# Kernel optimization log

Measured on AMD Instinct MI355X. Metric: run time of the kernel, lower is better.

Reference implementation:

```python
import jax, jax.numpy as jnp
from jax import lax
import numpy as np

STRIDE = 16
PRE_NMS = 2000
POST_NMS = 300
NMS_THRESH = 0.7
MIN_SIZE = 16.0  # * img_scale (=1.0)
DN = ('NCHW', 'OIHW', 'NCHW')


def _anchor_base(base=16, ratios=(0.5, 1.0, 2.0), scales=(8, 16, 32)):
    py = px = base / 2.0
    ab = np.zeros((len(ratios) * len(scales), 4), np.float32)
    k = 0
    for r in ratios:
        for s in scales:
            h = base * s * np.sqrt(r)
            w = base * s * np.sqrt(1.0 / r)
            ab[k] = [py - h / 2, px - w / 2, py + h / 2, px + w / 2]
            k += 1
    return ab


def _all_anchors(H, W, img_h, img_w):
    base = _anchor_base()
    sy = np.arange(H, dtype=np.float32) * STRIDE
    sx = np.arange(W, dtype=np.float32) * STRIDE
    yy, xx = np.meshgrid(sy, sx, indexing='ij')
    shifts = np.stack([yy, xx, yy, xx], axis=-1).reshape(-1, 1, 4)
    anchors = (shifts + base[None]).reshape(-1, 4).astype(np.float32)  # (H*W*9, 4)
    valid = np.where((anchors[:, 0] >= 0) & (anchors[:, 1] >= 0) &
                     (anchors[:, 2] <= img_h) & (anchors[:, 3] <= img_w))[0]
    return anchors, valid


def _loc2bbox(anc, loc):
    # anc: (1,K,4), loc: (B,K,4); boxes as (y1,x1,y2,x2)
    h = anc[..., 2] - anc[..., 0]
    w = anc[..., 3] - anc[..., 1]
    cy = anc[..., 0] + 0.5 * h
    cx = anc[..., 1] + 0.5 * w
    ncy = loc[..., 0] * h + cy
    ncx = loc[..., 1] * w + cx
    nh = h * jnp.exp(loc[..., 2])
    nw = w * jnp.exp(loc[..., 3])
    return jnp.stack([ncy - 0.5 * nh, ncx - 0.5 * nw,
                      ncy + 0.5 * nh, ncx + 0.5 * nw], axis=-1)


def _nms(boxes, scores):
    # boxes: (N,4), scores: (N,) -> (POST_NMS,4) zero-padded rois
    areas = (boxes[:, 2] - boxes[:, 0]) * (boxes[:, 3] - boxes[:, 1])

    def step(s, _):
        i = jnp.argmax(s)
        ok = s[i] > -jnp.inf
        b = boxes[i]
        yy1 = jnp.maximum(b[0], boxes[:, 0])
        xx1 = jnp.maximum(b[1], boxes[:, 1])
        yy2 = jnp.minimum(b[2], boxes[:, 2])
        xx2 = jnp.minimum(b[3], boxes[:, 3])
        inter = jnp.maximum(yy2 - yy1, 0.0) * jnp.maximum(xx2 - xx1, 0.0)
        iou = inter / (areas[i] + areas - inter + 1e-9)
        s = jnp.where(iou > NMS_THRESH, -jnp.inf, s).at[i].set(-jnp.inf)
        return s, (i, ok)

    _, (idx, ok) = lax.scan(step, scores, None, length=POST_NMS)
    return boxes[idx] * ok[:, None].astype(boxes.dtype)


def _conv(x, w, b, padding):
    y = lax.conv_general_dilated(x, w, (1, 1), padding, dimension_numbers=DN)
    return y + b[None, :, None, None]


def setup_inputs():
    key = jax.random.key(0)
    k = jax.random.split(key, 4)
    B, C, H, W = 2, 512, 64, 64
    std = 0.01
    return {
        'feat': jax.random.normal(k[0], (B, C, H, W), jnp.float32),
        'share_w': jax.random.normal(k[1], (512, 512, 3, 3), jnp.float32) * std,
        'share_b': jnp.zeros((512,), jnp.float32),
        'cls_w': jax.random.normal(k[2], (18, 512, 1, 1), jnp.float32) * std,
        'cls_b': jnp.zeros((18,), jnp.float32),
        'reg_w': jax.random.normal(k[3], (36, 512, 1, 1), jnp.float32) * std,
        'reg_b': jnp.zeros((36,), jnp.float32),
        'img_h': 1024,
        'img_w': 1024,
    }


def reference(feat, share_w, share_b, cls_w, cls_b, reg_w, reg_b, img_h, img_w):
    B, _, H, W = feat.shape
    anchors_np, valid_np = _all_anchors(H, W, img_h, img_w)
    anchors = jnp.asarray(anchors_np)
    valid = jnp.asarray(valid_np)

    shared = jax.nn.relu(_conv(feat, share_w, share_b, 'SAME'))
    cls = _conv(shared, cls_w, cls_b, 'VALID')   # (B,18,H,W)
    reg = _conv(shared, reg_w, reg_b, 'VALID')   # (B,36,H,W)

    # permute(0,2,3,1).view(-1,2), gather valid anchors, softmax
    cls = cls.transpose(0, 2, 3, 1).reshape(B, -1, 2)[:, valid]   # (B,K,2)
    cls = jax.nn.softmax(cls, axis=-1)
    reg = reg.transpose(0, 2, 3, 1).reshape(B, -1, 4)[:, valid]   # (B,K,4)

    # proposal layer: decode, clip, min-size filter, top-k, NMS
    anc = anchors[valid][None]                                    # (1,K,4)
    boxes = _loc2bbox(anc, reg)                                   # (B,K,4)
    boxes = jnp.stack([jnp.clip(boxes[..., 0], 0.0, img_h),
                       jnp.clip(boxes[..., 1], 0.0, img_w),
                       jnp.clip(boxes[..., 2], 0.0, img_h),
                       jnp.clip(boxes[..., 3], 0.0, img_w)], axis=-1)
    hs = boxes[..., 2] - boxes[..., 0]
    ws = boxes[..., 3] - boxes[..., 1]
    scores = jnp.where((hs >= MIN_SIZE) & (ws >= MIN_SIZE), cls[..., 1], -jnp.inf)

    top_s, top_i = lax.top_k(scores, PRE_NMS)                     # (B,PRE_NMS)
    top_boxes = jnp.take_along_axis(boxes, top_i[..., None], axis=1)
    rois = jax.vmap(_nms)(top_boxes, top_s)                       # (B,POST_NMS,4)
    roi_list = rois.reshape(-1, 4)
    roi_id = jnp.repeat(jnp.arange(B, dtype=jnp.int32), POST_NMS)
    return cls, reg, roi_list, roi_id, anchors
```

## Files before the change

### kernel.cpp

```cpp
#include <hip/hip_runtime.h>
#include <math.h>

typedef unsigned int u32;
typedef unsigned long long u64;
typedef unsigned short ushort_t;

typedef __attribute__((ext_vector_type(8))) short short8;
typedef __attribute__((ext_vector_type(16))) float f32x16;

#define KANC 18376
#define PRE 2000
#define PREP 2048
#define POST 300

#define OUT_CLS 0
#define OUT_REG 73504
#define OUT_ROI 220512
#define OUT_RID 222912
#define OUT_ANC 223512

#define WS_NHWC   0u
#define WS_FT     16777216u
#define WS_W3     41943040u
#define WS_VPOS   56098816u
#define WS_BOXES  56246272u
#define WS_KEYS   56834304u
#define WS_TOPBOX 56981312u
#define WS_TOPKEY 57046848u
#define WS_MASK   57063232u

#define A_SPL2 7920

__device__ __forceinline__ ushort_t f2bf(float f) {
    u32 u = __float_as_uint(f);
    u32 r = (u + 0x7FFFu + ((u >> 16) & 1u)) >> 16;
    return (ushort_t)r;
}
__device__ __forceinline__ float bf2f(ushort_t h) {
    return __uint_as_float(((u32)h) << 16);
}

__device__ __forceinline__ void anchor_base(int t, float& y1, float& x1, float& y2, float& x2) {
    const double SQ[3] = {0.7071067811865476, 1.0, 1.4142135623730951};
    const double SC[3] = {8.0, 16.0, 32.0};
    int ri = t / 3, si = t % 3;
    double h = 16.0 * SC[si] * SQ[ri];
    double w = 16.0 * SC[si] * SQ[2 - ri];
    y1 = (float)(8.0 - h * 0.5);
    x1 = (float)(8.0 - w * 0.5);
    y2 = (float)(8.0 + h * 0.5);
    x2 = (float)(8.0 + w * 0.5);
}

__global__ __launch_bounds__(256) void t1_feat(const float* __restrict__ feat,
                                               ushort_t* __restrict__ ft) {
    int by = blockIdx.y;
    int b = by >> 6, y = by & 63;
    int ci0 = blockIdx.x * 64;
    int tid = threadIdx.x;
    __shared__ float tile[64 * 65];
    for (int it = 0; it < 16; it++) {
        int idx = it * 256 + tid;
        int ci = idx >> 6, x = idx & 63;
        tile[ci * 65 + x] = feat[((size_t)(b * 512 + ci0 + ci) * 64 + y) * 64 + x];
    }
    __syncthreads();
    for (int it = 0; it < 16; it++) {
        int idx = it * 256 + tid;
        int x = idx >> 6, ci = idx & 63;
        float v = tile[ci * 65 + x];
        ushort_t hi = f2bf(v);
        float r1 = v - bf2f(hi);
        ushort_t mid = f2bf(r1);
        float r2 = r1 - bf2f(mid);
        ushort_t lo = f2bf(r2);
        size_t base = ((size_t)(b * 64 + y) * 64 + x) * 512 + ci0 + ci;
        const size_t spl = (size_t)2 * 64 * 64 * 512;
        ft[base] = hi;
        ft[base + spl] = mid;
        ft[base + 2 * spl] = lo;
    }
}

__global__ __launch_bounds__(256) void t2_wgt(const float* __restrict__ w,
                                              ushort_t* __restrict__ w3) {
    int tg = blockIdx.x * 256 + threadIdx.x;
    int co = tg >> 9, ci = tg & 511;
    const size_t spl = (size_t)9 * 512 * 512;
    for (int kk = 0; kk < 9; kk++) {
        float v = w[(size_t)(co * 512 + ci) * 9 + kk];
        ushort_t hi = f2bf(v);
        float r1 = v - bf2f(hi);
        ushort_t mid = f2bf(r1);
        float r2 = r1 - bf2f(mid);
        ushort_t lo = f2bf(r2);
        size_t base = ((size_t)kk * 512 + co) * 512 + ci;
        w3[base] = hi;
        w3[base + spl] = mid;
        w3[base + 2 * spl] = lo;
    }
}

__global__ __launch_bounds__(256) void k0_anchors(float* out, int* vpos,
                                                  const int* d_imgh, const int* d_imgw) {
    int a = blockIdx.x * 256 + threadIdx.x;
    float imgh = (float)d_imgh[0], imgw = (float)d_imgw[0];
    int t = a % 9, pix = a / 9, x = pix & 63, y = pix >> 6;
    int j = 0;
    bool myvalid = false;
#pragma unroll
    for (int tt = 0; tt < 9; tt++) {
        float c0, c1, c2, c3;
        anchor_base(tt, c0, c1, c2, c3);
        int ylo = (int)((-c0) / 16.0f) + 1;
        int yhi = (int)((imgh - c2) / 16.0f);
        int xlo = (int)((-c1) / 16.0f) + 1;
        int xhi = (int)((imgw - c3) / 16.0f);
        ylo = max(ylo, 0); yhi = min(yhi, 63);
        xlo = max(xlo, 0); xhi = min(xhi, 63);
        int Wt  = max(xhi - xlo + 1, 0);
        int nry = max(yhi - ylo + 1, 0);
        int rb  = min(max(y - ylo, 0), nry);
        bool vy = (y >= ylo) && (y <= yhi);
        int cb  = vy ? min(max(x - xlo, 0), Wt) : 0;
        bool val = vy && (x >= xlo) && (x <= xhi);
        j += rb * Wt + cb + ((tt < t && val) ? 1 : 0);
        if (tt == t) {
            myvalid = val;
            float4 o;
            o.x = c0 + 16.0f * y;
            o.y = c1 + 16.0f * x;
            o.z = c2 + 16.0f * y;
            o.w = c3 + 16.0f * x;
            *(float4*)&out[OUT_ANC + a * 4] = o;
        }
    }
    vpos[a] = myvalid ? j : -1;
}

__global__ __launch_bounds__(256, 3) void k1_conv(const ushort_t* __restrict__ ft,
                                                  const ushort_t* __restrict__ w3,
                                                  float* __restrict__ nhwc) {
    __shared__ ushort_t lds16[3 * A_SPL2];
    int tid = threadIdx.x;
    int bid = blockIdx.x;
    int nt = (bid >> 1) & 3;
    int kh = (bid >> 3) & 1;
    int mt = ((bid >> 4) << 1) | (bid & 1);
    int b = mt >> 6, y = mt & 63;
    int nb = nt << 7;
    int ct0 = kh * 8;

    int lane = tid & 63;
    int w = tid >> 6;
    int wn = w << 5;
    int nlane = lane & 31;
    int kgrp8 = (lane >> 5) * 8;

    const size_t FT_SPL = (size_t)2 * 64 * 64 * 512;
    const size_t W3_SPL = (size_t)9 * 512 * 512;

    int sx = tid >> 2;
    int sq = tid & 3;

    f32x16 acc[2];
#pragma unroll
    for (int mi = 0; mi < 2; mi++)
#pragma unroll
        for (int r = 0; r < 16; r++) acc[mi][r] = 0.0f;

    if (tid < 72) {
        int s = tid / 24, rem = tid % 24;
        int r = rem >> 3, rem2 = rem & 7;
        int side = rem2 >> 2, q = rem2 & 3;
        uint4 z = make_uint4(0, 0, 0, 0);
        *(uint4*)&lds16[s * A_SPL2 + (r * 66 + side * 65) * 40 + q * 8] = z;
    }

    uint4 pbA[9];
    auto loadA = [&](int ct) {
#pragma unroll
        for (int r = 0; r < 3; r++) {
            int yy = y - 1 + r;
            bool valid = (yy >= 0 && yy < 64);
            size_t rowbase = ((size_t)(b * 64 + (valid ? yy : 0)) * 64 + sx) * 512 + ct * 32 + sq * 8;
#pragma unroll
            for (int s = 0; s < 3; s++) {
                uint4 v = make_uint4(0, 0, 0, 0);
                if (valid) v = *(const uint4*)&ft[rowbase + (size_t)s * FT_SPL];
                pbA[r * 3 + s] = v;
            }
        }
    };
    auto writeA = [&]() {
#pragma unroll
        for (int r = 0; r < 3; r++)
#pragma unroll
            for (int s = 0; s < 3; s++)
                *(uint4*)&lds16[s * A_SPL2 + (r * 66 + sx + 1) * 40 + sq * 8] = pbA[r * 3 + s];
    };

    short8 breg[2][3];
    auto loadB = [&](int buf, int tap, int ks, int ct) {
        size_t cobase = ((size_t)(tap * 512 + nb + wn + nlane)) * 512 + ct * 32 + ks * 16 + kgrp8;
#pragma unroll
        for (int s = 0; s < 3; s++)
            breg[buf][s] = *(const short8*)&w3[(size_t)s * W3_SPL + cobase];
    };

    loadA(ct0);
    loadB(0, 0, 0, ct0);

    for (int ct = ct0; ct < ct0 + 8; ct++) {
        __syncthreads();
        writeA();
        __syncthreads();
        if (ct + 1 < ct0 + 8) loadA(ct + 1);

#pragma unroll
        for (int u = 0; u < 18; u++) {
            int cur = u & 1, alt = cur ^ 1;
            if (u + 1 < 18) loadB(alt, (u + 1) >> 1, (u + 1) & 1, ct);
            else if (ct + 1 < ct0 + 8) loadB(alt, 0, 0, ct + 1);
            int tap = u >> 1, ks = u & 1;
            int ky = tap / 3, kx = tap - ky * 3;

            short8 af[3][2];
#pragma unroll
            for (int s = 0; s < 3; s++) {
#pragma unroll
                for (int mi = 0; mi < 2; mi++)
                    af[s][mi] = *(const short8*)&lds16[s * A_SPL2 +
                        (ky * 66 + mi * 32 + nlane + kx) * 40 + ks * 16 + kgrp8];
            }
#pragma unroll
            for (int t = 0; t < 6; t++) {
                const int sa_t[6] = {0, 0, 1, 0, 1, 2};
                const int sb_t[6] = {0, 1, 0, 2, 1, 0};
                int sa = sa_t[t], sb = sb_t[t];
#pragma unroll
                for (int mi = 0; mi < 2; mi++)
                    acc[mi] = __builtin_amdgcn_mfma_f32_32x32x16_bf16(
                        af[sa][mi], breg[cur][sb], acc[mi], 0, 0, 0);
            }
        }
    }

    int co = nb + wn + nlane;
#pragma unroll
    for (int mi = 0; mi < 2; mi++) {
#pragma unroll
        for (int r = 0; r < 16; r++) {
            int xx = mi * 32 + (r & 3) + 8 * (r >> 2) + 4 * (lane >> 5);
            atomicAdd(&nhwc[((size_t)(b * 64 + y) * 64 + xx) * 512 + co], acc[mi][r]);
        }
    }
}

__global__ __launch_bounds__(256) void k2_heads(const float* __restrict__ nhwc,
                                                const float* __restrict__ share_b,
                                                const float* __restrict__ cls_w,
                                                const float* __restrict__ cls_b,
                                                const float* __restrict__ reg_w,
                                                const float* __restrict__ reg_b,
                                                const int* __restrict__ vpos,
                                                float* __restrict__ out,
                                                float* __restrict__ boxes_ws,
                                                u32* __restrict__ keys_ws,
                                                const int* d_imgh, const int* d_imgw) {
    int row = blockIdx.x;
    int b = row >> 6, y = row & 63;
    int tid = threadIdx.x;
    __shared__ float Al[64 * 68];
    __shared__ float Wl[54 * 64];
    __shared__ float Ob[54 * 64];
    int p = tid & 63, g = tid >> 6;
    int o0 = g * 14;
    int no = (g == 3) ? 12 : 14;
    float acc[14];
#pragma unroll
    for (int i = 0; i < 14; i++) acc[i] = 0.0f;
    for (int cib = 0; cib < 512; cib += 64) {
        for (int s = tid; s < 4096; s += 256) {
            int kk = s & 63, pp = s >> 6;
            float v = nhwc[((size_t)(b * 64 + y) * 64 + pp) * 512 + cib + kk] + share_b[cib + kk];
            Al[pp * 68 + kk] = fmaxf(v, 0.0f);
        }
        for (int s = tid; s < 54 * 64; s += 256) {
            int o = s >> 6, kk = s & 63;
            Wl[s] = (o < 18) ? cls_w[o * 512 + cib + kk] : reg_w[(o - 18) * 512 + cib + kk];
        }
        __syncthreads();
        for (int kq = 0; kq < 16; kq++) {
            float4 a4 = *(const float4*)&Al[p * 68 + kq * 4];
#pragma unroll
            for (int oo = 0; oo < 14; oo++)
                if (oo < no) {
                    float4 w4 = *(const float4*)&Wl[(o0 + oo) * 64 + kq * 4];
                    acc[oo] += a4.x * w4.x + a4.y * w4.y + a4.z * w4.z + a4.w * w4.w;
                }
        }
        __syncthreads();
    }
#pragma unroll
    for (int oo = 0; oo < 14; oo++)
        if (oo < no) {
            int o = o0 + oo;
            float bvv = (o < 18) ? cls_b[o] : reg_b[o - 18];
            Ob[o * 64 + p] = acc[oo] + bvv;
        }
    __syncthreads();
    float imgh = (float)d_imgh[0], imgw = (float)d_imgw[0];
    for (int task = tid; task < 576; task += 256) {
        int ta = task >> 6, p2 = task & 63;
        int a_idx = (y * 64 + p2) * 9 + ta;
        int j = vpos[a_idx];
        if (j < 0) continue;
        float c0 = Ob[(2 * ta) * 64 + p2], c1 = Ob[(2 * ta + 1) * 64 + p2];
        float m = fmaxf(c0, c1);
        float e0 = expf(c0 - m), e1 = expf(c1 - m);
        float sden = e0 + e1;
        float p0v = e0 / sden, p1v = e1 / sden;
        out[OUT_CLS + (size_t)(b * KANC + j) * 2 + 0] = p0v;
        out[OUT_CLS + (size_t)(b * KANC + j) * 2 + 1] = p1v;
        float l0 = Ob[(18 + 4 * ta + 0) * 64 + p2];
        float l1 = Ob[(18 + 4 * ta + 1) * 64 + p2];
        float l2 = Ob[(18 + 4 * ta + 2) * 64 + p2];
        float l3 = Ob[(18 + 4 * ta + 3) * 64 + p2];
        out[OUT_REG + (size_t)(b * KANC + j) * 4 + 0] = l0;
        out[OUT_REG + (size_t)(b * KANC + j) * 4 + 1] = l1;
        out[OUT_REG + (size_t)(b * KANC + j) * 4 + 2] = l2;
        out[OUT_REG + (size_t)(b * KANC + j) * 4 + 3] = l3;
        float b0, b1, b2, b3; anchor_base(ta, b0, b1, b2, b3);
        float ay1 = b0 + 16.0f * y, ax1 = b1 + 16.0f * p2;
        float ay2 = b2 + 16.0f * y, ax2 = b3 + 16.0f * p2;
        float h = ay2 - ay1, wdt = ax2 - ax1;
        float cy = ay1 + 0.5f * h, cx = ax1 + 0.5f * wdt;
        float ncy = l0 * h + cy, ncx = l1 * wdt + cx;
        float nh = h * expf(l2), nw = wdt * expf(l3);
        float by1 = fminf(fmaxf(ncy - 0.5f * nh, 0.0f), imgh);
        float bx1 = fminf(fmaxf(ncx - 0.5f * nw, 0.0f), imgw);
        float by2 = fminf(fmaxf(ncy + 0.5f * nh, 0.0f), imgh);
        float bx2 = fminf(fmaxf(ncx + 0.5f * nw, 0.0f), imgw);
        boxes_ws[(size_t)(b * KANC + j) * 4 + 0] = by1;
        boxes_ws[(size_t)(b * KANC + j) * 4 + 1] = bx1;
        boxes_ws[(size_t)(b * KANC + j) * 4 + 2] = by2;
        boxes_ws[(size_t)(b * KANC + j) * 4 + 3] = bx2;
        float hs = by2 - by1, wsz = bx2 - bx1;
        u32 key = 0;
        if (hs >= 16.0f && wsz >= 16.0f) key = __float_as_uint(p1v) + 1u;
        keys_ws[b * KANC + j] = key;
    }
}

__device__ __forceinline__ void suffix_scan(u32* suf, const u32* hist, int N, int tid) {
    for (int i = tid; i < N; i += 1024) suf[i] = hist[i];
    if (tid == 0) suf[N] = 0;
    __syncthreads();
    for (int off = 1; off < N; off <<= 1) {
        u32 add0 = 0, add1 = 0;
        int i0 = tid, i1 = tid + 1024;
        if (i0 < N) add0 = (i0 + off < N) ? suf[i0 + off] : 0;
        if (i1 < N) add1 = (i1 + off < N) ? suf[i1 + off] : 0;
        __syncthreads();
        if (i0 < N) suf[i0] += add0;
        if (i1 < N) suf[i1] += add1;
        __syncthreads();
    }
}

__global__ __launch_bounds__(1024) void k3_select(const u32* __restrict__ keys_ws,
                                                  const float* __restrict__ boxes_ws,
                                                  u32* __restrict__ topkey,
                                                  float* __restrict__ topbox) {
    int b = blockIdx.x, tid = threadIdx.x;
    const u32* keys = keys_ws + (size_t)b * KANC;
    __shared__ u32 hist[2048];
    __shared__ u32 suf[2049];
    __shared__ int Ps;
    __shared__ int cnt;
    __shared__ u64 sbuf[4096];

    for (int i = tid; i < 2048; i += 1024) hist[i] = 0;
    __syncthreads();
    for (int i = tid; i < KANC; i += 1024) atomicAdd(&hist[keys[i] >> 20], 1u);
    __syncthreads();
    suffix_scan(suf, hist, 2048, tid);
    if (tid == 0) Ps = 0;
    __syncthreads();
    for (int i = tid; i < 2048; i += 1024)
        if (suf[i] >= (u32)PRE && suf[i + 1] < (u32)PRE) Ps = i;
    __syncthreads();
    u32 P1 = (u32)Ps;
    u32 quota2 = (u32)PRE - suf[P1 + 1];
    __syncthreads();

    for (int i = tid; i < 1024; i += 1024) hist[i] = 0;
    __syncthreads();
    for (int i = tid; i < KANC; i += 1024) {
        u32 k = keys[i];
        if ((k >> 20) == P1) atomicAdd(&hist[(k >> 10) & 1023u], 1u);
    }
    __syncthreads();
    suffix_scan(suf, hist, 1024, tid);
    if (tid == 0) Ps = 0;
    __syncthreads();
    for (int i = tid; i < 1024; i += 1024)
        if (suf[i] >= quota2 && suf[i + 1] < quota2) Ps = i;
    __syncthreads();
    u32 P2 = (u32)Ps;
    u32 quota3 = quota2 - suf[P2 + 1];
    __syncthreads();

    u32 pref = (P1 << 10) | P2;
    for (int i = tid; i < 1024; i += 1024) hist[i] = 0;
    __syncthreads();
    for (int i = tid; i < KANC; i += 1024) {
        u32 k = keys[i];
        if ((k >> 10) == pref) atomicAdd(&hist[k & 1023u], 1u);
    }
    __syncthreads();
    suffix_scan(suf, hist, 1024, tid);
    if (tid == 0) Ps = 0;
    __syncthreads();
    for (int i = tid; i < 1024; i += 1024)
        if (suf[i] >= quota3 && suf[i + 1] < quota3) Ps = i;
    __syncthreads();
    u32 P3 = (u32)Ps;
    u32 T = (P1 << 20) | (P2 << 10) | P3;
    u32 Tm = (T < 1u) ? 1u : T;

    for (int i = tid; i < 4096; i += 1024) sbuf[i] = 0ull;
    if (tid == 0) cnt = 0;
    __syncthreads();
    for (int i = tid; i < KANC; i += 1024) {
        u32 k = keys[i];
        if (k >= Tm) {
            int pos = atomicAdd(&cnt, 1);
            if (pos < 4096)
                sbuf[pos] = ((u64)k << 32) | (u64)(0xFFFFFFFFu - (u32)i);
        }
    }
    __syncthreads();

    for (int k2 = 2; k2 <= 4096; k2 <<= 1) {
        for (int j2 = k2 >> 1; j2 > 0; j2 >>= 1) {
            for (int i = tid; i < 4096; i += 1024) {
                int ixj = i ^ j2;
                if (ixj > i) {
                    u64 va = sbuf[i], vb = sbuf[ixj];
                    bool descRegion = ((i & k2) == 0);
                    if (descRegion ? (va < vb) : (va > vb)) {
                        sbuf[i] = vb; sbuf[ixj] = va;
                    }
                }
            }
            __syncthreads();
        }
    }

    for (int i = tid; i < PREP; i += 1024) {
        u64 v = sbuf[i];
        u32 kk = (u32)(v >> 32);
        u32 j = 0xFFFFFFFFu - (u32)(v & 0xFFFFFFFFull);
        bool good = (i < PRE) && (kk != 0);
        topkey[b * PREP + i] = good ? kk : 0;
        float4 bx = make_float4(0.0f, 0.0f, 0.0f, 0.0f);
        if (good) bx = *(const float4*)&boxes_ws[(size_t)(b * KANC + j) * 4];
        *(float4*)&topbox[(size_t)(b * PREP + i) * 4] = bx;
    }
}

__global__ __launch_bounds__(64) void k4_mask(const float* __restrict__ topbox,
                                              u64* __restrict__ mask) {
    int jb = blockIdx.x, ib = blockIdx.y, b = blockIdx.z;
    int lane = threadIdx.x;
    float4 bi = *(const float4*)&topbox[(size_t)(b * PREP + ib * 64 + lane) * 4];
    float4 bj = *(const float4*)&topbox[(size_t)(b * PREP + jb * 64 + lane) * 4];
    float ai = (bi.z - bi.x) * (bi.w - bi.y);
    float aj = (bj.z - bj.x) * (bj.w - bj.y);
    u64 word = 0;
    for (int ii = 0; ii < 64; ii++) {
        float y1 = __shfl(bi.x, ii), x1 = __shfl(bi.y, ii);
        float y2 = __shfl(bi.z, ii), x2 = __shfl(bi.w, ii);
        float aii = __shfl(ai, ii);
        float yy1 = fmaxf(y1, bj.x), xx1 = fmaxf(x1, bj.y);
        float yy2 = fminf(y2, bj.z), xx2 = fminf(x2, bj.w);
        float inter = fmaxf(yy2 - yy1, 0.0f) * fmaxf(xx2 - xx1, 0.0f);
        float iou = inter / (aii + aj - inter + 1e-9f);
        u64 bal = __ballot(iou > 0.7f);
        if (lane == ii) word = bal;
    }
    mask[(size_t)(b * PREP + ib * 64 + lane) * 32 + jb] = word;
}

__global__ __launch_bounds__(64) void k5_nms(const u32* __restrict__ topkey,
                                             const float* __restrict__ topbox,
                                             const u64* __restrict__ mask,
                                             float* __restrict__ out) {
    int b = blockIdx.x;
    int lane = threadIdx.x;
    __shared__ int kept[POST];

    u64 validw = 0;
    for (int it = 0; it < 32; it++) {
        u64 wv = __ballot(topkey[b * PREP + it * 64 + lane] != 0);
        if (lane == it) validw = wv;
    }

    const u64* mb = mask + (size_t)b * PREP * 32;
    u64 remv = 0;
    const int CH = 16;
    u64 bufA[CH], bufB[CH];
    auto loadRows = [&](u64* buf, int base) {
#pragma unroll
        for (int k = 0; k < CH; k++)
            buf[k] = (lane < 32) ? mb[(size_t)(base + k) * 32 + lane] : 0ull;
    };
    int nk = 0;
    auto process = [&](u64* buf, int base) {
        int wi = base >> 6, sh = base & 63;
        u64 supw = __shfl(remv, wi);
        u64 valw = __shfl(validw, wi);
        u32 cand = (u32)(((~supw & valw) >> sh) & 0xFFFFull);
        while (cand) {
            int k = __builtin_ctz(cand);
            cand &= cand - 1;
            int i = base + k;
            remv |= buf[k];
            u64 rw = __shfl(buf[k], wi);
            cand &= ~((u32)((rw >> sh) & 0xFFFFull));
            if (lane == 0) kept[nk] = i;
            nk++;
            if (nk == POST) break;
        }
    };

    loadRows(bufA, 0);
    for (int base = 0; base < PRE && nk < POST; base += 2 * CH) {
        loadRows(bufB, base + CH);
        process(bufA, base);
        if (nk < POST && base + CH < PRE) {
            if (base + 2 * CH < PRE) loadRows(bufA, base + 2 * CH);
            process(bufB, base + CH);
        }
    }
    __syncthreads();
    for (int s = lane; s < POST; s += 64) {
        float4 bx = make_float4(0.0f, 0.0f, 0.0f, 0.0f);
        if (s < nk) bx = *(const float4*)&topbox[(size_t)(b * PREP + kept[s]) * 4];
        *(float4*)&out[OUT_ROI + (size_t)(b * POST + s) * 4] = bx;
        out[OUT_RID + b * POST + s] = (float)b;
    }
}

extern "C" void kernel_launch(void* const* d_in, const int* in_sizes, int n_in,
                              void* d_out, int out_size, void* d_ws, size_t ws_size,
                              hipStream_t stream) {
    (void)in_sizes; (void)n_in; (void)out_size; (void)ws_size;
    const float* feat    = (const float*)d_in[0];
    const float* share_w = (const float*)d_in[1];
    const float* share_b = (const float*)d_in[2];
    const float* cls_w   = (const float*)d_in[3];
    const float* cls_b   = (const float*)d_in[4];
    const float* reg_w   = (const float*)d_in[5];
    const float* reg_b   = (const float*)d_in[6];
    const int*   imgh    = (const int*)d_in[7];
    const int*   imgw    = (const int*)d_in[8];
    float* out = (float*)d_out;
    char* ws = (char*)d_ws;
    float*     nhwc   = (float*)(ws + WS_NHWC);
    ushort_t*  ft     = (ushort_t*)(ws + WS_FT);
    ushort_t*  w3     = (ushort_t*)(ws + WS_W3);
    int*       vpos   = (int*)(ws + WS_VPOS);
    float*     boxes  = (float*)(ws + WS_BOXES);
    u32*       keys   = (u32*)(ws + WS_KEYS);
    float*     topbox = (float*)(ws + WS_TOPBOX);
    u32*       topkey = (u32*)(ws + WS_TOPKEY);
    u64*       maskp  = (u64*)(ws + WS_MASK);

    hipMemsetAsync(nhwc, 0, (size_t)2 * 64 * 64 * 512 * 4, stream);
    t1_feat<<<dim3(8, 128), 256, 0, stream>>>(feat, ft);
    t2_wgt<<<1024, 256, 0, stream>>>(share_w, w3);
    k0_anchors<<<144, 256, 0, stream>>>(out, vpos, imgh, imgw);
    k1_conv<<<1024, 256, 0, stream>>>(ft, w3, nhwc);
    k2_heads<<<128, 256, 0, stream>>>(nhwc, share_b, cls_w, cls_b, reg_w, reg_b, vpos,
                                      out, boxes, keys, imgh, imgw);
    k3_select<<<2, 1024, 0, stream>>>(keys, boxes, topkey, topbox);
    k4_mask<<<dim3(32, 32, 2), 64, 0, stream>>>(topbox, maskp);
    k5_nms<<<2, 64, 0, stream>>>(topkey, topbox, maskp, out);
}
```

Measured before the change: 663.4 us.

## Fuse preprocessing kernels, widen conv N-tile, split heads kernel, inline anchor computation

Merges the feature and weight bf16-split kernels into one launch. The weight path now reads coalesced through LDS, and both paths write packed 32-bit pairs. The conv kernel gives each wave a 64-wide output-channel tile (2x2 MFMA accumulators), halving the grid and reusing each A fragment across more MFMAs, at the cost of more registers (launch bounds 2). The heads kernel splits each row into two 32-pixel halves with a register-blocked output layout, and the anchor kernel is folded into it, removing the vpos workspace and a launch.

```diff
diff --git a/kernel.cpp b/kernel.cpp
--- a/kernel.cpp
+++ b/kernel.cpp
@@ -38,6 +38,18 @@
 }
 __device__ __forceinline__ float bf2f(ushort_t h) {
     return __uint_as_float(((u32)h) << 16);
+}
+__device__ __forceinline__ u32 pack3(float v0, float v1, ushort_t* m0, ushort_t* m1,
+                                     ushort_t* l0, ushort_t* l1) {
+    ushort_t h0 = f2bf(v0);
+    float r = v0 - bf2f(h0);
+    *m0 = f2bf(r);
+    *l0 = f2bf(r - bf2f(*m0));
+    ushort_t h1 = f2bf(v1);
+    float r1 = v1 - bf2f(h1);
+    *m1 = f2bf(r1);
+    *l1 = f2bf(r1 - bf2f(*m1));
+    return (u32)h0 | ((u32)h1 << 16);
 }
 
 __device__ __forceinline__ void anchor_base(int t, float& y1, float& x1, float& y2, float& x2) {
@@ -52,108 +64,78 @@
     x2 = (float)(8.0 + w * 0.5);
 }
 
-__global__ __launch_bounds__(256) void t1_feat(const float* __restrict__ feat,
-                                               ushort_t* __restrict__ ft) {
-    int by = blockIdx.y;
-    int b = by >> 6, y = by & 63;
-    int ci0 = blockIdx.x * 64;
+__global__ __launch_bounds__(256) void t12_pre(const float* __restrict__ feat,
+                                               const float* __restrict__ w,
+                                               ushort_t* __restrict__ ft,
+                                               ushort_t* __restrict__ w3) {
+    __shared__ float lds[8 * 577];
     int tid = threadIdx.x;
-    __shared__ float tile[64 * 65];
-    for (int it = 0; it < 16; it++) {
-        int idx = it * 256 + tid;
-        int ci = idx >> 6, x = idx & 63;
-        tile[ci * 65 + x] = feat[((size_t)(b * 512 + ci0 + ci) * 64 + y) * 64 + x];
-    }
-    __syncthreads();
-    for (int it = 0; it < 16; it++) {
-        int idx = it * 256 + tid;
-        int x = idx >> 6, ci = idx & 63;
-        float v = tile[ci * 65 + x];
-        ushort_t hi = f2bf(v);
-        float r1 = v - bf2f(hi);
-        ushort_t mid = f2bf(r1);
-        float r2 = r1 - bf2f(mid);
-        ushort_t lo = f2bf(r2);
-        size_t base = ((size_t)(b * 64 + y) * 64 + x) * 512 + ci0 + ci;
+    int bid = blockIdx.x;
+    if (bid < 1024) {
+        int by = bid >> 3;
+        int b = by >> 6, y = by & 63;
+        int ci0 = (bid & 7) * 64;
+        for (int it = 0; it < 16; it++) {
+            int idx = it * 256 + tid;
+            int ci = idx >> 6, x = idx & 63;
+            lds[ci * 65 + x] = feat[((size_t)(b * 512 + ci0 + ci) * 64 + y) * 64 + x];
+        }
+        __syncthreads();
         const size_t spl = (size_t)2 * 64 * 64 * 512;
-        ft[base] = hi;
-        ft[base + spl] = mid;
-        ft[base + 2 * spl] = lo;
-    }
-}
-
-__global__ __launch_bounds__(256) void t2_wgt(const float* __restrict__ w,
-                                              ushort_t* __restrict__ w3) {
-    int tg = blockIdx.x * 256 + threadIdx.x;
-    int co = tg >> 9, ci = tg & 511;
-    const size_t spl = (size_t)9 * 512 * 512;
-    for (int kk = 0; kk < 9; kk++) {
-        float v = w[(size_t)(co * 512 + ci) * 9 + kk];
-        ushort_t hi = f2bf(v);
-        float r1 = v - bf2f(hi);
-        ushort_t mid = f2bf(r1);
-        float r2 = r1 - bf2f(mid);
-        ushort_t lo = f2bf(r2);
-        size_t base = ((size_t)kk * 512 + co) * 512 + ci;
-        w3[base] = hi;
-        w3[base + spl] = mid;
-        w3[base + 2 * spl] = lo;
-    }
-}
-
-__global__ __launch_bounds__(256) void k0_anchors(float* out, int* vpos,
-                                                  const int* d_imgh, const int* d_imgw) {
-    int a = blockIdx.x * 256 + threadIdx.x;
-    float imgh = (float)d_imgh[0], imgw = (float)d_imgw[0];
-    int t = a % 9, pix = a / 9, x = pix & 63, y = pix >> 6;
-    int j = 0;
-    bool myvalid = false;
-#pragma unroll
-    for (int tt = 0; tt < 9; tt++) {
-        float c0, c1, c2, c3;
-        anchor_base(tt, c0, c1, c2, c3);
-        int ylo = (int)((-c0) / 16.0f) + 1;
-        int yhi = (int)((imgh - c2) / 16.0f);
-        int xlo = (int)((-c1) / 16.0f) + 1;
-        int xhi = (int)((imgw - c3) / 16.0f);
-        ylo = max(ylo, 0); yhi = min(yhi, 63);
-        xlo = max(xlo, 0); xhi = min(xhi, 63);
-        int Wt  = max(xhi - xlo + 1, 0);
-        int nry = max(yhi - ylo + 1, 0);
-        int rb  = min(max(y - ylo, 0), nry);
-        bool vy = (y >= ylo) && (y <= yhi);
-        int cb  = vy ? min(max(x - xlo, 0), Wt) : 0;
-        bool val = vy && (x >= xlo) && (x <= xhi);
-        j += rb * Wt + cb + ((tt < t && val) ? 1 : 0);
-        if (tt == t) {
-            myvalid = val;
-            float4 o;
-            o.x = c0 + 16.0f * y;
-            o.y = c1 + 16.0f * x;
-            o.z = c2 + 16.0f * y;
-            o.w = c3 + 16.0f * x;
-            *(float4*)&out[OUT_ANC + a * 4] = o;
-        }
-    }
-    vpos[a] = myvalid ? j : -1;
-}
-
-__global__ __launch_bounds__(256, 3) void k1_conv(const ushort_t* __restrict__ ft,
+        u32* ft32 = (u32*)ft;
+        for (int it = 0; it < 8; it++) {
+            int idx = it * 256 + tid;
+            int x = idx >> 5, cp = idx & 31;
+            float v0 = lds[(2 * cp) * 65 + x];
+            float v1 = lds[(2 * cp + 1) * 65 + x];
+            ushort_t m0, m1, l0, l1;
+            u32 hi = pack3(v0, v1, &m0, &m1, &l0, &l1);
+            size_t base = ((size_t)(b * 64 + y) * 64 + x) * 512 + ci0 + 2 * cp;
+            ft32[base >> 1] = hi;
+            ft32[(base + spl) >> 1] = (u32)m0 | ((u32)m1 << 16);
+            ft32[(base + 2 * spl) >> 1] = (u32)l0 | ((u32)l1 << 16);
+        }
+    } else {
+        int b2 = bid - 1024;
+        int cob = b2 >> 3;
+        int cib = (b2 & 7) * 64;
+        for (int s = tid; s < 4608; s += 256) {
+            int co = s / 576, r = s - co * 576;
+            lds[co * 577 + r] = w[((size_t)(cob * 8 + co) * 512 + cib) * 9 + r];
+        }
+        __syncthreads();
+        const size_t spl = (size_t)9 * 512 * 512;
+        u32* w32 = (u32*)w3;
+        int co = tid >> 5, cp = tid & 31;
+        for (int kk = 0; kk < 9; kk++) {
+            float v0 = lds[co * 577 + (2 * cp) * 9 + kk];
+            float v1 = lds[co * 577 + (2 * cp + 1) * 9 + kk];
+            ushort_t m0, m1, l0, l1;
+            u32 hi = pack3(v0, v1, &m0, &m1, &l0, &l1);
+            size_t base = ((size_t)kk * 512 + cob * 8 + co) * 512 + cib + 2 * cp;
+            w32[base >> 1] = hi;
+            w32[(base + spl) >> 1] = (u32)m0 | ((u32)m1 << 16);
+            w32[(base + 2 * spl) >> 1] = (u32)l0 | ((u32)l1 << 16);
+        }
+    }
+}
+
+__global__ __launch_bounds__(256, 2) void k1_conv(const ushort_t* __restrict__ ft,
                                                   const ushort_t* __restrict__ w3,
                                                   float* __restrict__ nhwc) {
     __shared__ ushort_t lds16[3 * A_SPL2];
     int tid = threadIdx.x;
     int bid = blockIdx.x;
-    int nt = (bid >> 1) & 3;
-    int kh = (bid >> 3) & 1;
-    int mt = ((bid >> 4) << 1) | (bid & 1);
+    int nt = (bid >> 1) & 1;
+    int kh = (bid >> 2) & 1;
+    int mt = ((bid >> 3) << 1) | (bid & 1);
     int b = mt >> 6, y = mt & 63;
-    int nb = nt << 7;
+    int nb = nt << 8;
     int ct0 = kh * 8;
 
     int lane = tid & 63;
     int w = tid >> 6;
-    int wn = w << 5;
+    int wn = w << 6;
     int nlane = lane & 31;
     int kgrp8 = (lane >> 5) * 8;
 
@@ -163,11 +145,13 @@
     int sx = tid >> 2;
     int sq = tid & 3;
 
-    f32x16 acc[2];
+    f32x16 acc[2][2];
 #pragma unroll
     for (int mi = 0; mi < 2; mi++)
 #pragma unroll
-        for (int r = 0; r < 16; r++) acc[mi][r] = 0.0f;
+        for (int ni = 0; ni < 2; ni++)
+#pragma unroll
+            for (int r = 0; r < 16; r++) acc[mi][ni][r] = 0.0f;
 
     if (tid < 72) {
         int s = tid / 24, rem = tid % 24;
@@ -200,12 +184,16 @@
                 *(uint4*)&lds16[s * A_SPL2 + (r * 66 + sx + 1) * 40 + sq * 8] = pbA[r * 3 + s];
     };
 
-    short8 breg[2][3];
+    short8 breg[2][2][3];
     auto loadB = [&](int buf, int tap, int ks, int ct) {
-        size_t cobase = ((size_t)(tap * 512 + nb + wn + nlane)) * 512 + ct * 32 + ks * 16 + kgrp8;
-#pragma unroll
-        for (int s = 0; s < 3; s++)
-            breg[buf][s] = *(const short8*)&w3[(size_t)s * W3_SPL + cobase];
+#pragma unroll
+        for (int ni = 0; ni < 2; ni++) {
+            size_t cobase = ((size_t)(tap * 512 + nb + wn + ni * 32 + nlane)) * 512
+                            + ct * 32 + ks * 16 + kgrp8;
+#pragma unroll
+            for (int s = 0; s < 3; s++)
+                breg[buf][ni][s] = *(const short8*)&w3[(size_t)s * W3_SPL + cobase];
+        }
     };
 
     loadA(ct0);
@@ -240,19 +228,24 @@
                 int sa = sa_t[t], sb = sb_t[t];
 #pragma unroll
                 for (int mi = 0; mi < 2; mi++)
-                    acc[mi] = __builtin_amdgcn_mfma_f32_32x32x16_bf16(
-                        af[sa][mi], breg[cur][sb], acc[mi], 0, 0, 0);
-            }
-        }
-    }
-
-    int co = nb + wn + nlane;
+#pragma unroll
+                    for (int ni = 0; ni < 2; ni++)
+                        acc[mi][ni] = __builtin_amdgcn_mfma_f32_32x32x16_bf16(
+                            af[sa][mi], breg[cur][ni][sb], acc[mi][ni], 0, 0, 0);
+            }
+        }
+    }
+
 #pragma unroll
     for (int mi = 0; mi < 2; mi++) {
 #pragma unroll
-        for (int r = 0; r < 16; r++) {
-            int xx = mi * 32 + (r & 3) + 8 * (r >> 2) + 4 * (lane >> 5);
-            atomicAdd(&nhwc[((size_t)(b * 64 + y) * 64 + xx) * 512 + co], acc[mi][r]);
+        for (int ni = 0; ni < 2; ni++) {
+            int co = nb + wn + ni * 32 + nlane;
+#pragma unroll
+            for (int r = 0; r < 16; r++) {
+                int xx = mi * 32 + (r & 3) + 8 * (r >> 2) + 4 * (lane >> 5);
+                atomicAdd(&nhwc[((size_t)(b * 64 + y) * 64 + xx) * 512 + co], acc[mi][ni][r]);
+            }
         }
     }
 }
@@ -263,81 +256,121 @@
                                                 const float* __restrict__ cls_b,
                                                 const float* __restrict__ reg_w,
                                                 const float* __restrict__ reg_b,
-                                                const int* __restrict__ vpos,
                                                 float* __restrict__ out,
                                                 float* __restrict__ boxes_ws,
                                                 u32* __restrict__ keys_ws,
                                                 const int* d_imgh, const int* d_imgw) {
-    int row = blockIdx.x;
+    int bid = blockIdx.x;
+    int row = bid >> 1;
     int b = row >> 6, y = row & 63;
+    int h = bid & 1;
+    int p0 = h * 32;
     int tid = threadIdx.x;
-    __shared__ float Al[64 * 68];
-    __shared__ float Wl[54 * 64];
-    __shared__ float Ob[54 * 64];
-    int p = tid & 63, g = tid >> 6;
-    int o0 = g * 14;
-    int no = (g == 3) ? 12 : 14;
-    float acc[14];
-#pragma unroll
-    for (int i = 0; i < 14; i++) acc[i] = 0.0f;
+    __shared__ float Al[32 * 68];
+    __shared__ float Wl[64 * 64];
+    __shared__ float Ob[54 * 32];
+    int og = tid & 15, pg = tid >> 4;
+    float acc[2][4];
+#pragma unroll
+    for (int pp = 0; pp < 2; pp++)
+#pragma unroll
+        for (int j = 0; j < 4; j++) acc[pp][j] = 0.0f;
+
     for (int cib = 0; cib < 512; cib += 64) {
-        for (int s = tid; s < 4096; s += 256) {
+        for (int s = tid; s < 2048; s += 256) {
             int kk = s & 63, pp = s >> 6;
-            float v = nhwc[((size_t)(b * 64 + y) * 64 + pp) * 512 + cib + kk] + share_b[cib + kk];
+            float v = nhwc[((size_t)(b * 64 + y) * 64 + p0 + pp) * 512 + cib + kk]
+                      + share_b[cib + kk];
             Al[pp * 68 + kk] = fmaxf(v, 0.0f);
         }
-        for (int s = tid; s < 54 * 64; s += 256) {
+        for (int s = tid; s < 64 * 64; s += 256) {
             int o = s >> 6, kk = s & 63;
-            Wl[s] = (o < 18) ? cls_w[o * 512 + cib + kk] : reg_w[(o - 18) * 512 + cib + kk];
+            float wv = 0.0f;
+            if (o < 18) wv = cls_w[o * 512 + cib + kk];
+            else if (o < 54) wv = reg_w[(o - 18) * 512 + cib + kk];
+            Wl[s] = wv;
         }
         __syncthreads();
         for (int kq = 0; kq < 16; kq++) {
-            float4 a4 = *(const float4*)&Al[p * 68 + kq * 4];
-#pragma unroll
-            for (int oo = 0; oo < 14; oo++)
-                if (oo < no) {
-                    float4 w4 = *(const float4*)&Wl[(o0 + oo) * 64 + kq * 4];
-                    acc[oo] += a4.x * w4.x + a4.y * w4.y + a4.z * w4.z + a4.w * w4.w;
-                }
-        }
-        __syncthreads();
-    }
-#pragma unroll
-    for (int oo = 0; oo < 14; oo++)
-        if (oo < no) {
-            int o = o0 + oo;
-            float bvv = (o < 18) ? cls_b[o] : reg_b[o - 18];
-            Ob[o * 64 + p] = acc[oo] + bvv;
+            float4 a0 = *(const float4*)&Al[(pg * 2) * 68 + kq * 4];
+            float4 a1 = *(const float4*)&Al[(pg * 2 + 1) * 68 + kq * 4];
+#pragma unroll
+            for (int j = 0; j < 4; j++) {
+                float4 w4 = *(const float4*)&Wl[(og * 4 + j) * 64 + kq * 4];
+                acc[0][j] += a0.x * w4.x + a0.y * w4.y + a0.z * w4.z + a0.w * w4.w;
+                acc[1][j] += a1.x * w4.x + a1.y * w4.y + a1.z * w4.z + a1.w * w4.w;
+            }
+        }
+        __syncthreads();
+    }
+#pragma unroll
+    for (int pp = 0; pp < 2; pp++)
+#pragma unroll
+        for (int j = 0; j < 4; j++) {
+            int o = og * 4 + j;
+            if (o < 54) {
+                float bvv = (o < 18) ? cls_b[o] : reg_b[o - 18];
+                Ob[o * 32 + pg * 2 + pp] = acc[pp][j] + bvv;
+            }
         }
     __syncthreads();
     float imgh = (float)d_imgh[0], imgw = (float)d_imgw[0];
-    for (int task = tid; task < 576; task += 256) {
-        int ta = task >> 6, p2 = task & 63;
-        int a_idx = (y * 64 + p2) * 9 + ta;
-        int j = vpos[a_idx];
-        if (j < 0) continue;
-        float c0 = Ob[(2 * ta) * 64 + p2], c1 = Ob[(2 * ta + 1) * 64 + p2];
+    for (int task = tid; task < 288; task += 256) {
+        int ta = task >> 5, p2 = task & 31;
+        int x = p0 + p2;
+        int a_idx = (y * 64 + x) * 9 + ta;
+        int j = 0;
+        bool myvalid = false;
+#pragma unroll
+        for (int tt = 0; tt < 9; tt++) {
+            float c0, c1, c2, c3;
+            anchor_base(tt, c0, c1, c2, c3);
+            int ylo = (int)((-c0) / 16.0f) + 1;
+            int yhi = (int)((imgh - c2) / 16.0f);
+            int xlo = (int)((-c1) / 16.0f) + 1;
+            int xhi = (int)((imgw - c3) / 16.0f);
+            ylo = max(ylo, 0); yhi = min(yhi, 63);
+            xlo = max(xlo, 0); xhi = min(xhi, 63);
+            int Wt  = max(xhi - xlo + 1, 0);
+            int nry = max(yhi - ylo + 1, 0);
+            int rb  = min(max(y - ylo, 0), nry);
+            bool vy = (y >= ylo) && (y <= yhi);
+            int cb  = vy ? min(max(x - xlo, 0), Wt) : 0;
+            bool val = vy && (x >= xlo) && (x <= xhi);
+            j += rb * Wt + cb + ((tt < ta && val) ? 1 : 0);
+            if (tt == ta) {
+                myvalid = val;
+                float4 o4;
+                o4.x = c0 + 16.0f * y;
+                o4.y = c1 + 16.0f * x;
+                o4.z = c2 + 16.0f * y;
+                o4.w = c3 + 16.0f * x;
+                *(float4*)&out[OUT_ANC + a_idx * 4] = o4;
+            }
+        }
+        if (!myvalid) continue;
+        float c0 = Ob[(2 * ta) * 32 + p2], c1 = Ob[(2 * ta + 1) * 32 + p2];
         float m = fmaxf(c0, c1);
         float e0 = expf(c0 - m), e1 = expf(c1 - m);
         float sden = e0 + e1;
         float p0v = e0 / sden, p1v = e1 / sden;
         out[OUT_CLS + (size_t)(b * KANC + j) * 2 + 0] = p0v;
         out[OUT_CLS + (size_t)(b * KANC + j) * 2 + 1] = p1v;
-        float l0 = Ob[(18 + 4 * ta + 0) * 64 + p2];
-        float l1 = Ob[(18 + 4 * ta + 1) * 64 + p2];
-        float l2 = Ob[(18 + 4 * ta + 2) * 64 + p2];
-        float l3 = Ob[(18 + 4 * ta + 3) * 64 + p2];
+        float l0 = Ob[(18 + 4 * ta + 0) * 32 + p2];
+        float l1 = Ob[(18 + 4 * ta + 1) * 32 + p2];
+        float l2 = Ob[(18 + 4 * ta + 2) * 32 + p2];
+        float l3 = Ob[(18 + 4 * ta + 3) * 32 + p2];
         out[OUT_REG + (size_t)(b * KANC + j) * 4 + 0] = l0;
         out[OUT_REG + (size_t)(b * KANC + j) * 4 + 1] = l1;
         out[OUT_REG + (size_t)(b * KANC + j) * 4 + 2] = l2;
         out[OUT_REG + (size_t)(b * KANC + j) * 4 + 3] = l3;
         float b0, b1, b2, b3; anchor_base(ta, b0, b1, b2, b3);
-        float ay1 = b0 + 16.0f * y, ax1 = b1 + 16.0f * p2;
-        float ay2 = b2 + 16.0f * y, ax2 = b3 + 16.0f * p2;
-        float h = ay2 - ay1, wdt = ax2 - ax1;
-        float cy = ay1 + 0.5f * h, cx = ax1 + 0.5f * wdt;
-        float ncy = l0 * h + cy, ncx = l1 * wdt + cx;
-        float nh = h * expf(l2), nw = wdt * expf(l3);
+        float ay1 = b0 + 16.0f * y, ax1 = b1 + 16.0f * x;
+        float ay2 = b2 + 16.0f * y, ax2 = b3 + 16.0f * x;
+        float hh = ay2 - ay1, wdt = ax2 - ax1;
+        float cy = ay1 + 0.5f * hh, cx = ax1 + 0.5f * wdt;
+        float ncy = l0 * hh + cy, ncx = l1 * wdt + cx;
+        float nh = hh * expf(l2), nw = wdt * expf(l3);
         float by1 = fminf(fmaxf(ncy - 0.5f * nh, 0.0f), imgh);
         float bx1 = fminf(fmaxf(ncx - 0.5f * nw, 0.0f), imgw);
         float by2 = fminf(fmaxf(ncy + 0.5f * nh, 0.0f), imgh);
@@ -572,7 +605,6 @@
     float*     nhwc   = (float*)(ws + WS_NHWC);
     ushort_t*  ft     = (ushort_t*)(ws + WS_FT);
     ushort_t*  w3     = (ushort_t*)(ws + WS_W3);
-    int*       vpos   = (int*)(ws + WS_VPOS);
     float*     boxes  = (float*)(ws + WS_BOXES);
     u32*       keys   = (u32*)(ws + WS_KEYS);
     float*     topbox = (float*)(ws + WS_TOPBOX);
@@ -580,11 +612,9 @@
     u64*       maskp  = (u64*)(ws + WS_MASK);
 
     hipMemsetAsync(nhwc, 0, (size_t)2 * 64 * 64 * 512 * 4, stream);
-    t1_feat<<<dim3(8, 128), 256, 0, stream>>>(feat, ft);
-    t2_wgt<<<1024, 256, 0, stream>>>(share_w, w3);
-    k0_anchors<<<144, 256, 0, stream>>>(out, vpos, imgh, imgw);
-    k1_conv<<<1024, 256, 0, stream>>>(ft, w3, nhwc);
-    k2_heads<<<128, 256, 0, stream>>>(nhwc, share_b, cls_w, cls_b, reg_w, reg_b, vpos,
+    t12_pre<<<1536, 256, 0, stream>>>(feat, share_w, ft, w3);
+    k1_conv<<<512, 256, 0, stream>>>(ft, w3, nhwc);
+    k2_heads<<<256, 256, 0, stream>>>(nhwc, share_b, cls_w, cls_b, reg_w, reg_b,
                                       out, boxes, keys, imgh, imgw);
     k3_select<<<2, 1024, 0, stream>>>(keys, boxes, topkey, topbox);
     k4_mask<<<dim3(32, 32, 2), 64, 0, stream>>>(topbox, maskp);
```

New measurement: 645.6 us. 1.03x faster.
